# Kernel tuning notes

Hardware: AMD Instinct MI355X
Metric: run time of the kernel (lower is better)

## Reference

```python
import jax, jax.numpy as jnp
import numpy as np

B, T, V, C = 64, 256, 256, 4
NEG = -jnp.inf


def setup_inputs() -> dict:
    key = jax.random.key(0)
    k1, k2, k3 = jax.random.split(key, 3)
    logits = jax.random.normal(k1, (B, T, V, C), dtype=jnp.float32)
    ar_sent = jax.random.randint(k2, (B, T), 0, 61, dtype=jnp.int32)
    en_sent = jax.random.randint(k3, (B, V), 0, 61, dtype=jnp.int32)
    return {"logits": logits, "ar_sent": ar_sent, "en_sent": en_sent}


def _forward_alpha(ins, dele, sub):
    # ins/dele/sub: [B,T,V] log-scores of insertion/deletion/substitution into cell (t,v)
    b, t_len, v_len = ins.shape
    z = jnp.zeros((b, 1), ins.dtype)
    # row t=0: only insertions -> prefix sum
    alpha0 = jnp.concatenate([z, jnp.cumsum(ins[:, 0, 1:], axis=1)], axis=1)

    def step(prev, xs):
        ins_t, del_t, sub_t = xs  # each [B,V]
        # c[v]: contributions from previous row (deletion + substitution)
        c = jnp.concatenate(
            [del_t[:, :1] + prev[:, :1],
             jnp.logaddexp(del_t[:, 1:] + prev[:, 1:], sub_t[:, 1:] + prev[:, :-1])],
            axis=1)
        # within-row recurrence alpha[v] = logaddexp(ins[v]+alpha[v-1], c[v])
        # solved in closed form: alpha[v] = S[v] + logcumsumexp_k<=v (c[k]-S[k]), S=prefix sum of ins
        s = jnp.concatenate([z, jnp.cumsum(ins_t[:, 1:], axis=1)], axis=1)
        row = s + jax.lax.cumlogsumexp(c - s, axis=1)
        return row, row

    xs = (jnp.moveaxis(ins, 1, 0)[1:], jnp.moveaxis(dele, 1, 0)[1:], jnp.moveaxis(sub, 1, 0)[1:])
    _, rows = jax.lax.scan(step, alpha0, xs)
    return jnp.moveaxis(jnp.concatenate([alpha0[None], rows], axis=0), 0, 1)  # [B,T,V]


def _backward_beta(ins, dele, sub):
    b, t_len, v_len = ins.shape
    z = jnp.zeros((b, 1), ins.dtype)
    # row t=T-1: only insertions -> suffix sum, corner = 0
    ins_last = ins[:, -1, :]
    beta_last = jnp.concatenate([jnp.cumsum(ins_last[:, -2::-1], axis=1)[:, ::-1], z], axis=1)

    def step(nxt, xs):
        ins_t, del_t, sub_t = xs
        # c[v]: contributions from next row (deletion + substitution); v=V-1 has no substitution
        c = jnp.concatenate(
            [jnp.logaddexp(del_t[:, :-1] + nxt[:, :-1], sub_t[:, :-1] + nxt[:, 1:]),
             del_t[:, -1:] + nxt[:, -1:]],
            axis=1)
        # beta[v] = logaddexp(ins[v]+beta[v+1], c[v]): reverse linear recurrence -> flip + closed form
        fins = ins_t[:, ::-1]
        fc = c[:, ::-1]
        fs = jnp.concatenate([z, jnp.cumsum(fins[:, 1:], axis=1)], axis=1)
        fb = fs + jax.lax.cumlogsumexp(fc - fs, axis=1)
        row = fb[:, ::-1]
        return row, row

    xs = (jnp.moveaxis(ins, 1, 0)[:-1][::-1],
          jnp.moveaxis(dele, 1, 0)[:-1][::-1],
          jnp.moveaxis(sub, 1, 0)[:-1][::-1])
    _, rows = jax.lax.scan(step, beta_last, xs)
    beta = jnp.concatenate([rows[::-1], beta_last[None]], axis=0)
    return jnp.moveaxis(beta, 0, 1)  # [B,T,V]


def reference(logits, ar_sent, en_sent):
    # tiny_table class ids: deletion=0, insertion=1, substitution=2 (constant, char-independent)
    scores = jax.nn.log_softmax(logits, axis=3)  # [B,T,V,4]
    dele, ins, sub = scores[..., 0], scores[..., 1], scores[..., 2]
    alpha = _forward_alpha(ins, dele, sub)

    # beta / expected counts are computed under no_grad in the original
    sg = jax.lax.stop_gradient
    s = sg(scores)
    a = sg(alpha)
    beta = _backward_beta(s[..., 1], s[..., 0], s[..., 2])

    bsz, t_len, v_len, n_cls = scores.shape
    cls = jnp.arange(n_cls)[None, None, :]
    t_lt = (jnp.arange(t_len) < t_len - 1)[:, None, None]
    v_lt = (jnp.arange(v_len) < v_len - 1)[None, :, None]
    pd = jnp.broadcast_to(jnp.where((cls == 0) & t_lt, 0.0, NEG), (t_len, v_len, n_cls))
    pi = jnp.broadcast_to(jnp.where((cls == 1) & v_lt, 0.0, NEG), (t_len, v_len, n_cls))
    ps = jnp.broadcast_to(jnp.where((cls == 2) & t_lt & v_lt, 0.0, NEG), (t_len, v_len, n_cls))

    full = jnp.full((bsz, t_len, v_len, n_cls), NEG, scores.dtype)
    ed = full.at[:, 1:].set(a[:, :-1, :, None] + s[:, 1:] + pd[None, 1:] + beta[:, 1:, :, None])
    ei = full.at[:, :, 1:].set(a[:, :, :-1, None] + s[:, :, 1:] + pi[None, :, 1:] + beta[:, :, 1:, None])
    es = full.at[:, 1:, 1:].set(
        a[:, :-1, :-1, None] + s[:, 1:, 1:] + ps[None, 1:, 1:] + beta[:, 1:, 1:, None])

    ec = jnp.logaddexp(jnp.logaddexp(ed, ei), es)
    norm = jax.nn.logsumexp(ec, axis=3, keepdims=True)
    norm = jnp.where(jnp.isneginf(norm), 0.0, norm)  # avoid nan at degenerate (0,0)-type cells
    expected_counts = jnp.exp(ec - norm)
    return (scores, expected_counts, alpha[0, -1, -1])
```

## Files before the change

### kernel.cpp

```cpp
#include <hip/hip_runtime.h>
#include <math.h>

#define BB 64
#define TT 256
#define VV 256
#define SLABS 321
#define SLAB_F (SLABS * 256)
#define PLANE ((size_t)BB * SLAB_F)
#define NSLAB_W 319

typedef __attribute__((ext_vector_type(4))) _Float16 half4;

__device__ __forceinline__ float dpp_shr1_f(float x) {
    return __int_as_float(__builtin_amdgcn_update_dpp(
        __float_as_int(x), __float_as_int(x), 0x138, 0xF, 0xF, false));
}
__device__ __forceinline__ int dpp_shr1_i(int x) {
    return __builtin_amdgcn_update_dpp(x, x, 0x138, 0xF, 0xF, false);
}

__device__ __forceinline__ float lae2(float x, float y) {
    float m = fmaxf(x, y);
    float d = x - y;
    return m + __logf(1.0f + __expf(-fabsf(d)));
}

__global__ void __launch_bounds__(256) k_prep(const float4* __restrict__ lg,
                                              float4* __restrict__ sc,
                                              _Float16* __restrict__ Dd,
                                              _Float16* __restrict__ Di,
                                              _Float16* __restrict__ Du) {
    int blk = blockIdx.x;
    int b = blk / NSLAB_W;
    int s = blk - b * NSLAB_W;
    int v = threadIdx.x;
    int t = s - (v >> 2);
    bool valid = (t >= 0) && (t < TT);
    int tc = valid ? t : 0;
    size_t ci = ((size_t)b << 16) | ((size_t)tc << 8) | (size_t)v;
    float4 x = lg[ci];
    float m = fmaxf(fmaxf(x.x, x.y), fmaxf(x.z, x.w));
    float e0 = __expf(x.x - m), e1 = __expf(x.y - m);
    float e2 = __expf(x.z - m), e3 = __expf(x.w - m);
    float ssum = e0 + e1 + e2 + e3;
    float l = m + __logf(ssum);
    if (valid) sc[ci] = make_float4(x.x - l, x.y - l, x.z - l, x.w - l);
    float rcp = valid ? (1.0f / ssum) : 0.0f;
    size_t pb = (size_t)b * SLAB_F + ((size_t)s << 8) + v;
    Dd[pb] = (_Float16)(e0 * rcp);
    Di[pb] = (_Float16)(e1 * rcp);
    Du[pb] = (_Float16)(e2 * rcp);
}

__global__ void __launch_bounds__(64) k_dp(const _Float16* __restrict__ Pd,
                                           const _Float16* __restrict__ Pi,
                                           const _Float16* __restrict__ Pu,
                                           _Float16* __restrict__ W0,
                                           _Float16* __restrict__ W1,
                                           float* __restrict__ scalar_out) {
    const int b = blockIdx.x;
    const int lane = threadIdx.x;
    const bool l0 = (lane == 0);
    const size_t base = (size_t)b * SLAB_F + (lane << 2);

    const half4* __restrict__ pd = (const half4*)(Pd + base);
    const half4* __restrict__ pi = (const half4*)(Pi + base);
    const half4* __restrict__ pu = (const half4*)(Pu + base);
    half4* __restrict__ pw0 = (half4*)(W0 + base);
    half4* __restrict__ pw1 = (half4*)(W1 + base);
    const int SS = 64;

    half4 d0,d1,d2,d3,d4,d5,d6,d7;
    half4 i0,i1,i2,i3,i4,i5,i6,i7;
    half4 u0,u1,u2,u3,u4,u5,u6,u7;
    d0 = pd[0*SS]; i0 = pi[0*SS]; u0 = pu[0*SS];
    d1 = pd[1*SS]; i1 = pi[1*SS]; u1 = pu[1*SS];
    d2 = pd[2*SS]; i2 = pi[2*SS]; u2 = pu[2*SS];
    d3 = pd[3*SS]; i3 = pi[3*SS]; u3 = pu[3*SS];
    d4 = pd[4*SS]; i4 = pi[4*SS]; u4 = pu[4*SS];
    d5 = pd[5*SS]; i5 = pi[5*SS]; u5 = pu[5*SS];
    d6 = pd[6*SS]; i6 = pi[6*SS]; u6 = pu[6*SS];
    d7 = pd[7*SS]; i7 = pi[7*SS]; u7 = pu[7*SS];

    float A0 = 0.0f, A1 = 0.0f, A2 = 0.0f, A3 = 0.0f;
    int   E  = 0;
    float LC = 0.0f, LP = 0.0f;
    int   EC = 0,    EP = 0;
    float sA3 = 0.0f;
    int   sEn = 0;

    int s = 0;

#define STEP(DD, II, UU, FIXUP, CLAMP, CAP)                                       \
    {                                                                             \
        const half4 dl = DD, in = II, su = UU;                                    \
        {                                                                         \
            int sp = s + 8;                                                       \
            if (CLAMP) sp = sp > SLABS - 1 ? SLABS - 1 : sp;                      \
            DD = pd[sp * SS]; II = pi[sp * SS]; UU = pu[sp * SS];                 \
        }                                                                         \
        int E_eff = E;                                                            \
        bool isT0 = false;                                                        \
        if (FIXUP) {                                                              \
            isT0 = (s == lane);                                                   \
            E_eff = isT0 ? (l0 ? 0 : EC) : E;                                     \
        }                                                                         \
        const float lc = l0 ? 0.0f : ldexpf(LC, EC - E_eff);                      \
        const float lp = l0 ? 0.0f : ldexpf(LP, EP - E_eff);                      \
        float X0 = (float)dl.x * A0 + (float)su.x * lp;                           \
        float X1 = (float)dl.y * A1 + (float)su.y * A0;                           \
        float X2 = (float)dl.z * A2 + (float)su.z * A1;                           \
        float X3 = (float)dl.w * A3 + (float)su.w * A2;                           \
        if (FIXUP && isT0) {                                                      \
            X0 = l0 ? 1.0f : 0.0f; X1 = 0.0f; X2 = 0.0f; X3 = 0.0f;               \
        }                                                                         \
        const float iy = (float)in.y, iz = (float)in.z, iw = (float)in.w;         \
        const float B0 = X0;                                                      \
        const float B1 = fmaf(B0, iy, X1);                                        \
        const float B2 = fmaf(B1, iz, X2);                                        \
        const float B3 = fmaf(B2, iw, X3);                                        \
        const float Q0 = (float)in.x;                                             \
        const float Q1 = Q0 * iy;                                                 \
        const float Q2 = Q1 * iz;                                                 \
        const float Q3 = Q2 * iw;                                                 \
        float nA0 = fmaf(lc, Q0, B0);                                             \
        float nA1 = fmaf(lc, Q1, B1);                                             \
        float nA2 = fmaf(lc, Q2, B2);                                             \
        float nA3 = fmaf(lc, Q3, B3);                                             \
                           \
        const float r0 = __builtin_amdgcn_rcpf(nA0);                              \
        const float r1 = __builtin_amdgcn_rcpf(nA1);                              \
        const float r2 = __builtin_amdgcn_rcpf(nA2);                              \
        const float r3 = __builtin_amdgcn_rcpf(nA3);                              \
        half4 h0, h1;                                                             \
        h0.x = (_Float16)((float)dl.x * A0 * r0);                                 \
        h0.y = (_Float16)((float)dl.y * A1 * r1);                                 \
        h0.z = (_Float16)((float)dl.z * A2 * r2);                                 \
        h0.w = (_Float16)((float)dl.w * A3 * r3);                                 \
        h1.x = (_Float16)(Q0 * lc * r0);                                          \
        h1.y = (_Float16)(iy * nA0 * r1);                                         \
        h1.z = (_Float16)(iz * nA1 * r2);                                         \
        h1.w = (_Float16)(iw * nA2 * r3);                                         \
        pw0[s * SS] = h0;                                                         \
        pw1[s * SS] = h1;                                                         \
        const int eb = (int)((__float_as_uint(nA3) >> 23) & 255u) - 126;          \
        const int En = E_eff + eb;                                                \
        nA3 = ldexpf(nA3, -eb);                                                   \
        nA0 = ldexpf(nA0, -eb);                                                   \
        nA1 = ldexpf(nA1, -eb);                                                   \
        nA2 = ldexpf(nA2, -eb);                                                   \
        LP = LC; EP = EC;                                                         \
        LC = dpp_shr1_f(nA3);                                                     \
        EC = dpp_shr1_i(En);                                                      \
        if (CAP && s == TT + 62) { sA3 = nA3; sEn = En; }     \
        A0 = nA0; A1 = nA1; A2 = nA2; A3 = nA3; E = En;                           \
        ++s;                                                                      \
    }

#pragma unroll 1
    for (int it = 0; it < 8; ++it) {
        STEP(d0, i0, u0, 1, 0, 0);
        STEP(d1, i1, u1, 1, 0, 0);
        STEP(d2, i2, u2, 1, 0, 0);
        STEP(d3, i3, u3, 1, 0, 0);
        STEP(d4, i4, u4, 1, 0, 0);
        STEP(d5, i5, u5, 1, 0, 0);
        STEP(d6, i6, u6, 1, 0, 0);
        STEP(d7, i7, u7, 1, 0, 0);
    }
#pragma unroll 1
    for (int it = 0; it < 31; ++it) {
        STEP(d0, i0, u0, 0, 0, 0);
        STEP(d1, i1, u1, 0, 0, 0);
        STEP(d2, i2, u2, 0, 0, 0);
        STEP(d3, i3, u3, 0, 0, 0);
        STEP(d4, i4, u4, 0, 0, 0);
        STEP(d5, i5, u5, 0, 0, 0);
        STEP(d6, i6, u6, 0, 0, 0);
        STEP(d7, i7, u7, 0, 0, 0);
    }
    STEP(d0, i0, u0, 0, 1, 1);
    STEP(d1, i1, u1, 0, 1, 1);
    STEP(d2, i2, u2, 0, 1, 1);
    STEP(d3, i3, u3, 0, 1, 1);
    STEP(d4, i4, u4, 0, 1, 1);
    STEP(d5, i5, u5, 0, 1, 1);
    STEP(d6, i6, u6, 0, 1, 1);
    STEP(d7, i7, u7, 0, 1, 1);
#undef STEP

    if ((b == 0) && (lane == 63))
        scalar_out[0] = logf(sA3) + (float)sEn * 0.6931471805599453f;
}

__global__ void __launch_bounds__(256) k_wperm(const _Float16* __restrict__ W0,
                                               const _Float16* __restrict__ W1,
                                               float4* __restrict__ out) {
    int blk = blockIdx.x;
    int b = blk / NSLAB_W;
    int s = blk - b * NSLAB_W;
    int v = threadIdx.x;
    int g = v >> 2;
    int t = s - g;
    if ((t < 0) | (t >= TT)) return;

    size_t pb = (size_t)b * SLAB_F + ((size_t)s << 8) + v;
    float w0 = (float)W0[pb];
    float w1 = (float)W1[pb];
    w0 = fminf(fmaxf(w0, 0.0f), 1.0f);
    w1 = fminf(fmaxf(w1, 0.0f), 1.0f);
    float w2 = fmaxf(0.0f, 1.0f - w0 - w1);

    bool tE = (t == 0) | (t == TT - 1);
    bool vE = (v == 0) | (v == VV - 1);
    float4 o;
    o.x = tE ? 0.0f : (vE ? 1.0f : w0);
    o.y = vE ? 0.0f : (tE ? 1.0f : w1);
    o.z = (tE | vE) ? 0.0f : w2;
    o.w = 0.0f;
    out[((size_t)b << 16) | ((size_t)t << 8) | (size_t)v] = o;
}

__global__ void k_prep_legacy(const float4* __restrict__ lg, float4* __restrict__ sc, int n) {
    int i = blockIdx.x * blockDim.x + threadIdx.x;
    int st = gridDim.x * blockDim.x;
    for (; i < n; i += st) {
        float4 x = lg[i];
        float m = fmaxf(fmaxf(x.x, x.y), fmaxf(x.z, x.w));
        float s = __expf(x.x - m) + __expf(x.y - m) + __expf(x.z - m) + __expf(x.w - m);
        float l = m + __logf(s);
        sc[i] = make_float4(x.x - l, x.y - l, x.z - l, x.w - l);
    }
}
__global__ void __launch_bounds__(64) k_dp_legacy(const float4* __restrict__ scores,
                                                  float4* __restrict__ counts,
                                                  float* __restrict__ scalar_out) {
    const int b = blockIdx.x;
    const int lane = threadIdx.x;
    const int v0 = lane << 2;
    const float4* __restrict__ srow = scores + ((size_t)b * TT * VV + v0);
    float4* __restrict__ crow = counts + ((size_t)b * TT * VV + v0);
    float4 P0[4], P1[4], P2[4];
    {
        int r; const float4* p;
        r = 0 - lane; r = r < 0 ? 0 : r; p = srow + (size_t)r * VV;
        P0[0]=p[0]; P0[1]=p[1]; P0[2]=p[2]; P0[3]=p[3];
        r = 1 - lane; r = r < 0 ? 0 : r; p = srow + (size_t)r * VV;
        P1[0]=p[0]; P1[1]=p[1]; P1[2]=p[2]; P1[3]=p[3];
        r = 2 - lane; r = r < 0 ? 0 : r; p = srow + (size_t)r * VV;
        P2[0]=p[0]; P2[1]=p[1]; P2[2]=p[2]; P2[3]=p[3];
    }
    float aPrev[4] = { -INFINITY, -INFINITY, -INFINITY, -INFINITY };
    float leftPrev = -INFINITY, leftCur = -INFINITY;
    int s = 0;
#define STEPL(BUF)                                                                \
    {                                                                             \
        const int t = s - lane;                                                   \
        const bool active = (t >= 0) && (t < TT);                                 \
        float4 c0 = BUF[0], c1 = BUF[1], c2 = BUF[2], c3 = BUF[3];                \
        {                                                                         \
            int tp = t + 3; tp = tp < 0 ? 0 : tp; tp = tp > TT - 1 ? TT - 1 : tp; \
            const float4* lp = srow + (size_t)tp * VV;                            \
            BUF[0]=lp[0]; BUF[1]=lp[1]; BUF[2]=lp[2]; BUF[3]=lp[3];               \
        }                                                                         \
        float aPm1_0 = (lane == 0) ? -INFINITY : leftPrev;                        \
        float cv0 = lae2(c0.x + aPrev[0], c0.z + aPm1_0);                         \
        float cv1 = lae2(c1.x + aPrev[1], c1.z + aPrev[0]);                       \
        float cv2 = lae2(c2.x + aPrev[2], c2.z + aPrev[1]);                       \
        float cv3 = lae2(c3.x + aPrev[3], c3.z + aPrev[2]);                       \
        if (lane == 0) cv0 = c0.x + aPrev[0];                                     \
        if (t == 0) {                                                             \
            cv0 = (lane == 0) ? 0.0f : -INFINITY;                                 \
            cv1 = -INFINITY; cv2 = -INFINITY; cv3 = -INFINITY;                    \
        }                                                                         \
        float lc = (lane == 0) ? -INFINITY : leftCur;                             \
        float a0 = lae2(lc + c0.y, cv0);                                          \
        float a1 = lae2(a0 + c1.y, cv1);                                          \
        float a2 = lae2(a1 + c2.y, cv2);                                          \
        float a3 = lae2(a2 + c3.y, cv3);                                          \
        if (active) {                                                             \
            const bool tE = (t == 0) | (t == TT - 1);                             \
            float aCm1[4] = { lc, a0, a1, a2 };                                   \
            float aPm1[4] = { aPm1_0, aPrev[0], aPrev[1], aPrev[2] };             \
            float aP[4]   = { aPrev[0], aPrev[1], aPrev[2], aPrev[3] };           \
            float aA[4]   = { a0, a1, a2, a3 };                                   \
            float4 sv[4]  = { c0, c1, c2, c3 };                                   \
            float4* cp = crow + (size_t)t * VV;                                   \
            _Pragma("unroll")                                                     \
            for (int k = 0; k < 4; ++k) {                                         \
                const bool vE = (k == 0 && lane == 0) || (k == 3 && lane == 63);  \
                float w0 = __expf(aP[k]   + sv[k].x - aA[k]);                     \
                float w1 = __expf(aCm1[k] + sv[k].y - aA[k]);                     \
                float w2 = __expf(aPm1[k] + sv[k].z - aA[k]);                     \
                float4 o;                                                         \
                o.x = tE ? 0.0f : (vE ? 1.0f : w0);                               \
                o.y = vE ? 0.0f : (tE ? 1.0f : w1);                               \
                o.z = (tE || vE) ? 0.0f : w2;                                     \
                o.w = 0.0f;                                                       \
                cp[k] = o;                                                        \
            }                                                                     \
            if ((t == TT - 1) && (lane == 63) && (b == 0)) scalar_out[0] = a3;    \
        }                                                                         \
        aPrev[0]=a0; aPrev[1]=a1; aPrev[2]=a2; aPrev[3]=a3;                       \
        leftPrev = leftCur;                                                       \
        leftCur = __shfl_up(a3, 1);                                               \
        ++s;                                                                      \
    }
#pragma unroll 1
    for (int it = 0; it < 107; ++it) { STEPL(P0); STEPL(P1); STEPL(P2); }
#undef STEPL
}

extern "C" void kernel_launch(void* const* d_in, const int* in_sizes, int n_in,
                              void* d_out, int out_size, void* d_ws, size_t ws_size,
                              hipStream_t stream) {
    const float* logits = (const float*)d_in[0];
    float* out = (float*)d_out;
    const size_t ncell = (size_t)BB * TT * VV;

    float4* scores = (float4*)out;
    float4* counts = (float4*)(out + ncell * 4);
    float* scalar_out = out + ncell * 8;

    _Float16* Pd = (_Float16*)d_ws;
    _Float16* Pi = Pd + PLANE;
    _Float16* Pu = Pi + PLANE;
    _Float16* W0 = Pu + PLANE;
    _Float16* W1 = W0 + PLANE;

    size_t need = PLANE * 2 * 5;
    if (ws_size >= need) {
        k_prep<<<BB * NSLAB_W, 256, 0, stream>>>((const float4*)logits, scores, Pd, Pi, Pu);
        k_dp<<<BB, 64, 0, stream>>>(Pd, Pi, Pu, W0, W1, scalar_out);
        k_wperm<<<BB * NSLAB_W, 256, 0, stream>>>(W0, W1, counts);
    } else {
        k_prep_legacy<<<2048, 256, 0, stream>>>((const float4*)logits, scores, (int)ncell);
        k_dp_legacy<<<BB, 64, 0, stream>>>(scores, counts, scalar_out);
    }
}
```

Measured before the change: 105.3 us.

## Pack deletion/substitution probs as FP8 pair and interleave W outputs

```diff
diff --git a/kernel.cpp b/kernel.cpp
--- a/kernel.cpp
+++ b/kernel.cpp
@@ -10,6 +10,7 @@
 #define NSLAB_W 319
 
 typedef __attribute__((ext_vector_type(4))) _Float16 half4;
+typedef __attribute__((ext_vector_type(8))) _Float16 half8;
 
 __device__ __forceinline__ float dpp_shr1_f(float x) {
     return __int_as_float(__builtin_amdgcn_update_dpp(
@@ -27,9 +28,8 @@
 
 __global__ void __launch_bounds__(256) k_prep(const float4* __restrict__ lg,
                                               float4* __restrict__ sc,
-                                              _Float16* __restrict__ Dd,
-                                              _Float16* __restrict__ Di,
-                                              _Float16* __restrict__ Du) {
+                                              unsigned short* __restrict__ PDU,
+                                              _Float16* __restrict__ Pi) {
     int blk = blockIdx.x;
     int b = blk / NSLAB_W;
     int s = blk - b * NSLAB_W;
@@ -47,40 +47,35 @@
     if (valid) sc[ci] = make_float4(x.x - l, x.y - l, x.z - l, x.w - l);
     float rcp = valid ? (1.0f / ssum) : 0.0f;
     size_t pb = (size_t)b * SLAB_F + ((size_t)s << 8) + v;
-    Dd[pb] = (_Float16)(e0 * rcp);
-    Di[pb] = (_Float16)(e1 * rcp);
-    Du[pb] = (_Float16)(e2 * rcp);
-}
-
-__global__ void __launch_bounds__(64) k_dp(const _Float16* __restrict__ Pd,
+    int pk = __builtin_amdgcn_cvt_pk_fp8_f32(e0 * rcp, e2 * rcp, 0, false);
+    PDU[pb] = (unsigned short)pk;
+    Pi[pb] = (_Float16)(e1 * rcp);
+}
+
+__global__ void __launch_bounds__(64) k_dp(const unsigned short* __restrict__ PDU,
                                            const _Float16* __restrict__ Pi,
-                                           const _Float16* __restrict__ Pu,
-                                           _Float16* __restrict__ W0,
-                                           _Float16* __restrict__ W1,
+                                           _Float16* __restrict__ W,
                                            float* __restrict__ scalar_out) {
     const int b = blockIdx.x;
     const int lane = threadIdx.x;
     const bool l0 = (lane == 0);
-    const size_t base = (size_t)b * SLAB_F + (lane << 2);
-
-    const half4* __restrict__ pd = (const half4*)(Pd + base);
-    const half4* __restrict__ pi = (const half4*)(Pi + base);
-    const half4* __restrict__ pu = (const half4*)(Pu + base);
-    half4* __restrict__ pw0 = (half4*)(W0 + base);
-    half4* __restrict__ pw1 = (half4*)(W1 + base);
+    const size_t cellbase = (size_t)b * SLAB_F + (lane << 2);
+
+    const uint2* __restrict__ pdu = (const uint2*)(PDU + cellbase);
+    const half4* __restrict__ pi = (const half4*)(Pi + cellbase);
+    half8* __restrict__ pw = (half8*)(W + (size_t)b * SLABS * 512) + lane;
     const int SS = 64;
 
-    half4 d0,d1,d2,d3,d4,d5,d6,d7;
+    uint2 m0,m1,m2,m3,m4,m5,m6,m7;
     half4 i0,i1,i2,i3,i4,i5,i6,i7;
-    half4 u0,u1,u2,u3,u4,u5,u6,u7;
-    d0 = pd[0*SS]; i0 = pi[0*SS]; u0 = pu[0*SS];
-    d1 = pd[1*SS]; i1 = pi[1*SS]; u1 = pu[1*SS];
-    d2 = pd[2*SS]; i2 = pi[2*SS]; u2 = pu[2*SS];
-    d3 = pd[3*SS]; i3 = pi[3*SS]; u3 = pu[3*SS];
-    d4 = pd[4*SS]; i4 = pi[4*SS]; u4 = pu[4*SS];
-    d5 = pd[5*SS]; i5 = pi[5*SS]; u5 = pu[5*SS];
-    d6 = pd[6*SS]; i6 = pi[6*SS]; u6 = pu[6*SS];
-    d7 = pd[7*SS]; i7 = pi[7*SS]; u7 = pu[7*SS];
+    m0 = pdu[0*SS]; i0 = pi[0*SS];
+    m1 = pdu[1*SS]; i1 = pi[1*SS];
+    m2 = pdu[2*SS]; i2 = pi[2*SS];
+    m3 = pdu[3*SS]; i3 = pi[3*SS];
+    m4 = pdu[4*SS]; i4 = pi[4*SS];
+    m5 = pdu[5*SS]; i5 = pi[5*SS];
+    m6 = pdu[6*SS]; i6 = pi[6*SS];
+    m7 = pdu[7*SS]; i7 = pi[7*SS];
 
     float A0 = 0.0f, A1 = 0.0f, A2 = 0.0f, A3 = 0.0f;
     int   E  = 0;
@@ -91,14 +86,22 @@
 
     int s = 0;
 
-#define STEP(DD, II, UU, FIXUP, CLAMP, CAP)                                       \
+#define STEP(MM, II, FIXUP, CLAMP, CAP)                                           \
     {                                                                             \
-        const half4 dl = DD, in = II, su = UU;                                    \
+        const uint2 mw = MM; const half4 in = II;                                 \
         {                                                                         \
             int sp = s + 8;                                                       \
             if (CLAMP) sp = sp > SLABS - 1 ? SLABS - 1 : sp;                      \
-            DD = pd[sp * SS]; II = pi[sp * SS]; UU = pu[sp * SS];                 \
-        }                                                                         \
+            MM = pdu[sp * SS]; II = pi[sp * SS];                                  \
+        }                                                                         \
+        const float dlx = __builtin_amdgcn_cvt_f32_fp8((int)mw.x, 0);             \
+        const float sux = __builtin_amdgcn_cvt_f32_fp8((int)mw.x, 1);             \
+        const float dly = __builtin_amdgcn_cvt_f32_fp8((int)mw.x, 2);             \
+        const float suy = __builtin_amdgcn_cvt_f32_fp8((int)mw.x, 3);             \
+        const float dlz = __builtin_amdgcn_cvt_f32_fp8((int)mw.y, 0);             \
+        const float suz = __builtin_amdgcn_cvt_f32_fp8((int)mw.y, 1);             \
+        const float dlw = __builtin_amdgcn_cvt_f32_fp8((int)mw.y, 2);             \
+        const float suw = __builtin_amdgcn_cvt_f32_fp8((int)mw.y, 3);             \
         int E_eff = E;                                                            \
         bool isT0 = false;                                                        \
         if (FIXUP) {                                                              \
@@ -107,10 +110,10 @@
         }                                                                         \
         const float lc = l0 ? 0.0f : ldexpf(LC, EC - E_eff);                      \
         const float lp = l0 ? 0.0f : ldexpf(LP, EP - E_eff);                      \
-        float X0 = (float)dl.x * A0 + (float)su.x * lp;                           \
-        float X1 = (float)dl.y * A1 + (float)su.y * A0;                           \
-        float X2 = (float)dl.z * A2 + (float)su.z * A1;                           \
-        float X3 = (float)dl.w * A3 + (float)su.w * A2;                           \
+        float X0 = dlx * A0 + sux * lp;                                           \
+        float X1 = dly * A1 + suy * A0;                                           \
+        float X2 = dlz * A2 + suz * A1;                                           \
+        float X3 = dlw * A3 + suw * A2;                                           \
         if (FIXUP && isT0) {                                                      \
             X0 = l0 ? 1.0f : 0.0f; X1 = 0.0f; X2 = 0.0f; X3 = 0.0f;               \
         }                                                                         \
@@ -132,17 +135,16 @@
         const float r1 = __builtin_amdgcn_rcpf(nA1);                              \
         const float r2 = __builtin_amdgcn_rcpf(nA2);                              \
         const float r3 = __builtin_amdgcn_rcpf(nA3);                              \
-        half4 h0, h1;                                                             \
-        h0.x = (_Float16)((float)dl.x * A0 * r0);                                 \
-        h0.y = (_Float16)((float)dl.y * A1 * r1);                                 \
-        h0.z = (_Float16)((float)dl.z * A2 * r2);                                 \
-        h0.w = (_Float16)((float)dl.w * A3 * r3);                                 \
-        h1.x = (_Float16)(Q0 * lc * r0);                                          \
-        h1.y = (_Float16)(iy * nA0 * r1);                                         \
-        h1.z = (_Float16)(iz * nA1 * r2);                                         \
-        h1.w = (_Float16)(iw * nA2 * r3);                                         \
-        pw0[s * SS] = h0;                                                         \
-        pw1[s * SS] = h1;                                                         \
+        half8 hw;                                                                 \
+        hw[0] = (_Float16)(dlx * A0 * r0);                                        \
+        hw[1] = (_Float16)(dly * A1 * r1);                                        \
+        hw[2] = (_Float16)(dlz * A2 * r2);                                        \
+        hw[3] = (_Float16)(dlw * A3 * r3);                                        \
+        hw[4] = (_Float16)(Q0 * lc * r0);                                         \
+        hw[5] = (_Float16)(iy * nA0 * r1);                                        \
+        hw[6] = (_Float16)(iz * nA1 * r2);                                        \
+        hw[7] = (_Float16)(iw * nA2 * r3);                                        \
+        pw[s * 64] = hw;                                                          \
         const int eb = (int)((__float_as_uint(nA3) >> 23) & 255u) - 126;          \
         const int En = E_eff + eb;                                                \
         nA3 = ldexpf(nA3, -eb);                                                   \
@@ -159,54 +161,54 @@
 
 #pragma unroll 1
     for (int it = 0; it < 8; ++it) {
-        STEP(d0, i0, u0, 1, 0, 0);
-        STEP(d1, i1, u1, 1, 0, 0);
-        STEP(d2, i2, u2, 1, 0, 0);
-        STEP(d3, i3, u3, 1, 0, 0);
-        STEP(d4, i4, u4, 1, 0, 0);
-        STEP(d5, i5, u5, 1, 0, 0);
-        STEP(d6, i6, u6, 1, 0, 0);
-        STEP(d7, i7, u7, 1, 0, 0);
+        STEP(m0, i0, 1, 0, 0);
+        STEP(m1, i1, 1, 0, 0);
+        STEP(m2, i2, 1, 0, 0);
+        STEP(m3, i3, 1, 0, 0);
+        STEP(m4, i4, 1, 0, 0);
+        STEP(m5, i5, 1, 0, 0);
+        STEP(m6, i6, 1, 0, 0);
+        STEP(m7, i7, 1, 0, 0);
     }
 #pragma unroll 1
     for (int it = 0; it < 31; ++it) {
-        STEP(d0, i0, u0, 0, 0, 0);
-        STEP(d1, i1, u1, 0, 0, 0);
-        STEP(d2, i2, u2, 0, 0, 0);
-        STEP(d3, i3, u3, 0, 0, 0);
-        STEP(d4, i4, u4, 0, 0, 0);
-        STEP(d5, i5, u5, 0, 0, 0);
-        STEP(d6, i6, u6, 0, 0, 0);
-        STEP(d7, i7, u7, 0, 0, 0);
-    }
-    STEP(d0, i0, u0, 0, 1, 1);
-    STEP(d1, i1, u1, 0, 1, 1);
-    STEP(d2, i2, u2, 0, 1, 1);
-    STEP(d3, i3, u3, 0, 1, 1);
-    STEP(d4, i4, u4, 0, 1, 1);
-    STEP(d5, i5, u5, 0, 1, 1);
-    STEP(d6, i6, u6, 0, 1, 1);
-    STEP(d7, i7, u7, 0, 1, 1);
+        STEP(m0, i0, 0, 0, 0);
+        STEP(m1, i1, 0, 0, 0);
+        STEP(m2, i2, 0, 0, 0);
+        STEP(m3, i3, 0, 0, 0);
+        STEP(m4, i4, 0, 0, 0);
+        STEP(m5, i5, 0, 0, 0);
+        STEP(m6, i6, 0, 0, 0);
+        STEP(m7, i7, 0, 0, 0);
+    }
+    STEP(m0, i0, 0, 1, 1);
+    STEP(m1, i1, 0, 1, 1);
+    STEP(m2, i2, 0, 1, 1);
+    STEP(m3, i3, 0, 1, 1);
+    STEP(m4, i4, 0, 1, 1);
+    STEP(m5, i5, 0, 1, 1);
+    STEP(m6, i6, 0, 1, 1);
+    STEP(m7, i7, 0, 1, 1);
 #undef STEP
 
     if ((b == 0) && (lane == 63))
         scalar_out[0] = logf(sA3) + (float)sEn * 0.6931471805599453f;
 }
 
-__global__ void __launch_bounds__(256) k_wperm(const _Float16* __restrict__ W0,
-                                               const _Float16* __restrict__ W1,
+__global__ void __launch_bounds__(256) k_wperm(const _Float16* __restrict__ W,
                                                float4* __restrict__ out) {
     int blk = blockIdx.x;
     int b = blk / NSLAB_W;
     int s = blk - b * NSLAB_W;
     int v = threadIdx.x;
     int g = v >> 2;
+    int k = v & 3;
     int t = s - g;
     if ((t < 0) | (t >= TT)) return;
 
-    size_t pb = (size_t)b * SLAB_F + ((size_t)s << 8) + v;
-    float w0 = (float)W0[pb];
-    float w1 = (float)W1[pb];
+    size_t wb = (size_t)b * SLABS * 512 + ((size_t)s << 9) + ((size_t)g << 3) + k;
+    float w0 = (float)W[wb];
+    float w1 = (float)W[wb + 4];
     w0 = fminf(fmaxf(w0, 0.0f), 1.0f);
     w1 = fminf(fmaxf(w1, 0.0f), 1.0f);
     float w2 = fmaxf(0.0f, 1.0f - w0 - w1);
@@ -322,17 +324,15 @@
     float4* counts = (float4*)(out + ncell * 4);
     float* scalar_out = out + ncell * 8;
 
-    _Float16* Pd = (_Float16*)d_ws;
-    _Float16* Pi = Pd + PLANE;
-    _Float16* Pu = Pi + PLANE;
-    _Float16* W0 = Pu + PLANE;
-    _Float16* W1 = W0 + PLANE;
-
-    size_t need = PLANE * 2 * 5;
+    unsigned short* PDU = (unsigned short*)d_ws;
+    _Float16* Pi = (_Float16*)(PDU + PLANE);
+    _Float16* W  = (_Float16*)(Pi + PLANE);
+
+    size_t need = PLANE * 2 + PLANE * 2 + PLANE * 4;
     if (ws_size >= need) {
-        k_prep<<<BB * NSLAB_W, 256, 0, stream>>>((const float4*)logits, scores, Pd, Pi, Pu);
-        k_dp<<<BB, 64, 0, stream>>>(Pd, Pi, Pu, W0, W1, scalar_out);
-        k_wperm<<<BB * NSLAB_W, 256, 0, stream>>>(W0, W1, counts);
+        k_prep<<<BB * NSLAB_W, 256, 0, stream>>>((const float4*)logits, scores, PDU, Pi);
+        k_dp<<<BB, 64, 0, stream>>>(PDU, Pi, W, scalar_out);
+        k_wperm<<<BB * NSLAB_W, 256, 0, stream>>>(W, counts);
     } else {
         k_prep_legacy<<<2048, 256, 0, stream>>>((const float4*)logits, scores, (int)ncell);
         k_dp_legacy<<<BB, 64, 0, stream>>>(scores, counts, scalar_out);
```

Result: no change. 105.2 us (-0.1%).
